# Kernel optimization log

Hardware: AMD Instinct MI355X
Metric: run time of the kernel (lower is better)

The kernel has to match this reference:

```python
import jax, jax.numpy as jnp
import numpy as np

N, E, IN, OUT, ED, NT, H = 20000, 640000, 128, 256, 32, 16, 8
GATC = OUT // 2          # 128 per-layer GAT width
C = GATC // H            # 16 per-head dim
GINEC = OUT - GATC       # 128


def setup_inputs() -> dict:
    key = jax.random.key(0)
    ks = jax.random.split(key, 16)
    s = 0.05
    return {
        "x": jax.random.normal(ks[0], (N, IN), jnp.float32),
        "edge_index": jax.random.randint(ks[1], (2, E), 0, N, jnp.int64),
        "edge_attr": jax.random.normal(ks[2], (E, ED), jnp.float32),
        "edge_types": jax.random.randint(ks[3], (E,), 0, NT, jnp.int64),
        "gat_W": jax.random.normal(ks[4], (IN, H * C), jnp.float32) * s,
        "gat_b": jnp.zeros((H * C,), jnp.float32),
        "gat_edge_W": jax.random.normal(ks[5], (ED, H * C), jnp.float32) * s,
        "gat_a_src": jax.random.normal(ks[6], (H, C), jnp.float32) * s,
        "gat_a_dst": jax.random.normal(ks[7], (H, C), jnp.float32) * s,
        "gat_a_edge": jax.random.normal(ks[8], (H, C), jnp.float32) * s,
        "gat_type_emb": jax.random.normal(ks[9], (NT, ED), jnp.float32) * s,
        "gine_type_emb": jax.random.normal(ks[10], (NT, ED), jnp.float32) * s,
        "gine_edge_W": jax.random.normal(ks[11], (ED, IN), jnp.float32) * s,
        "gine_edge_b": jnp.zeros((IN,), jnp.float32),
        "gine_eps": jnp.zeros((1,), jnp.float32),
        "gine_W1": jax.random.normal(ks[12], (IN, GINEC), jnp.float32) * s,
        "gine_b1": jnp.zeros((GINEC,), jnp.float32),
        "gine_W2": jax.random.normal(ks[13], (GINEC, GINEC), jnp.float32) * s,
        "gine_b2": jnp.zeros((GINEC,), jnp.float32),
        "comb_W": jax.random.normal(ks[14], (H * C + GINEC, OUT), jnp.float32) * s,
        "comb_b": jnp.zeros((OUT,), jnp.float32),
        "ln_g": jnp.ones((OUT,), jnp.float32),
        "ln_b": jnp.zeros((OUT,), jnp.float32),
    }


def reference(x, edge_index, edge_attr, edge_types,
              gat_W, gat_b, gat_edge_W, gat_a_src, gat_a_dst, gat_a_edge,
              gat_type_emb, gine_type_emb, gine_edge_W, gine_edge_b, gine_eps,
              gine_W1, gine_b1, gine_W2, gine_b2, comb_W, comb_b, ln_g, ln_b):
    n = x.shape[0]
    h_, c_ = gat_a_src.shape
    src, dst = edge_index[0], edge_index[1]

    # ---- GAT branch (edge-featured multi-head attention) ----
    e = edge_attr + gat_type_emb[edge_types]                      # [E, ED]
    h = (x @ gat_W).reshape(n, h_, c_)                            # [N, H, C]
    ee = (e @ gat_edge_W).reshape(-1, h_, c_)                     # [E, H, C]
    a_s = jnp.einsum('nhc,hc->nh', h, gat_a_src)                  # [N, H]
    a_d = jnp.einsum('nhc,hc->nh', h, gat_a_dst)
    a_e = jnp.einsum('ehc,hc->eh', ee, gat_a_edge)                # [E, H]
    logit = jax.nn.leaky_relu(a_s[src] + a_d[dst] + a_e, 0.2)     # [E, H]
    # segment softmax over incoming edges of each destination node
    mx = jax.ops.segment_max(logit, dst, num_segments=n)
    p = jnp.exp(logit - mx[dst])
    denom = jax.ops.segment_sum(p, dst, num_segments=n)
    alpha = p / (denom[dst] + 1e-16)                              # [E, H]
    msg = alpha[:, :, None] * h[src]                              # [E, H, C]
    gat_out = jax.ops.segment_sum(msg, dst, num_segments=n).reshape(n, h_ * c_) + gat_b

    # ---- GINE branch ----
    ep = (edge_attr + gine_type_emb[edge_types]) @ gine_edge_W + gine_edge_b  # [E, IN]
    agg = jax.ops.segment_sum(jax.nn.relu(x[src] + ep), dst, num_segments=n)
    h2 = (1.0 + gine_eps[0]) * x + agg
    gine_out = jax.nn.relu(h2 @ gine_W1 + gine_b1) @ gine_W2 + gine_b2        # [N, GINEC]

    # ---- fuse: Linear + LayerNorm + ReLU (dropout is identity in eval) ----
    z = jnp.concatenate([gat_out, gine_out], axis=-1) @ comb_W + comb_b       # [N, OUT]
    mu = jnp.mean(z, axis=-1, keepdims=True)
    var = jnp.var(z, axis=-1, keepdims=True)
    z = (z - mu) * jax.lax.rsqrt(var + 1e-5) * ln_g + ln_b
    return jax.nn.relu(z)
```

## Files before the change

### kernel.cpp

```cpp
#include <hip/hip_runtime.h>

#define N_NODES 20000
#define N_EDGES 640000

typedef _Float16 h2v   __attribute__((ext_vector_type(2)));
typedef _Float16 h16x8 __attribute__((ext_vector_type(8)));
typedef float    f32x4v __attribute__((ext_vector_type(4)));
typedef unsigned u32x4v __attribute__((ext_vector_type(4)));

__device__ __forceinline__ unsigned packh2(float a, float b){
    h2v v; v.x = (_Float16)a; v.y = (_Float16)b;
    return __builtin_bit_cast(unsigned, v);
}

__global__ void k0_zero(float4* __restrict__ p, int n4){
    int i = blockIdx.x*blockDim.x + threadIdx.x;
    int stride = gridDim.x*blockDim.x;
    float4 z; z.x=0.f; z.y=0.f; z.z=0.f; z.w=0.f;
    for (; i<n4; i+=stride) p[i] = z;
}

__global__ void kD_detect(const int* __restrict__ eidx_w, const int* __restrict__ ety_w,
                          int* __restrict__ flags){
    int i = blockIdx.x*blockDim.x + threadIdx.x;
    int stride = gridDim.x*blockDim.x;
    int a0 = 0, a1 = 0;
    for (int w = 2*i+1; w < 2*N_EDGES; w += 2*stride) a0 |= eidx_w[w];
    for (int w = 2*i+1; w < N_EDGES;   w += 2*stride) a1 |= ety_w[w];
    if (a0) atomicOr(&flags[0], 1);
    if (a1) atomicOr(&flags[1], 1);
}

__global__ void kN_norm(const int* __restrict__ eidx_w, const int* __restrict__ ety_w,
                        const int* __restrict__ flags,
                        int* __restrict__ dst, int* __restrict__ srcty,
                        int* __restrict__ rankA, int* __restrict__ cnt){
    int i = blockIdx.x*blockDim.x + threadIdx.x;
    int stride = gridDim.x*blockDim.x;
    const bool e32 = (flags[0] != 0);
    const bool t32 = (flags[1] != 0);
    for (int e = i; e < N_EDGES; e += stride){
        int s, d, t;
        if (e32){ s = eidx_w[e];   d = eidx_w[N_EDGES + e]; }
        else    { s = eidx_w[2*e]; d = eidx_w[2*N_EDGES + 2*e]; }
        t = t32 ? ety_w[e] : ety_w[2*e];
        s = min(max(s, 0), N_NODES-1);
        d = min(max(d, 0), N_NODES-1);
        t = min(max(t, 0), 15);
        dst[e] = d; srcty[e] = s | (t << 20);
        rankA[e] = atomicAdd(&cnt[d], 1);
    }
}

__global__ __launch_bounds__(1024) void kS_scan(const int* __restrict__ cnt,
                                                int* __restrict__ row_ptr){
    __shared__ int sW[16];
    __shared__ int sWS[16];
    __shared__ int sbase;
    const int t = threadIdx.x, lane = t & 63, wv = t >> 6;
    if (t==0) sbase = 0;
    __syncthreads();
    for (int base=0; base<N_NODES; base+=4096){
        const int idx0 = base + t*4;
        int v0 = (idx0  <N_NODES) ? cnt[idx0  ] : 0;
        int v1 = (idx0+1<N_NODES) ? cnt[idx0+1] : 0;
        int v2 = (idx0+2<N_NODES) ? cnt[idx0+2] : 0;
        int v3 = (idx0+3<N_NODES) ? cnt[idx0+3] : 0;
        int p1 = v0+v1, p2 = p1+v2, tot = p2+v3;
        int xs = tot;
        #pragma unroll
        for (int off=1; off<64; off<<=1){
            int y = __shfl_up(xs, off, 64);
            if (lane >= off) xs += y;
        }
        if (lane==63) sW[wv] = xs;
        __syncthreads();
        if (t < 16){
            int wvv = sW[t], ws = wvv;
            #pragma unroll
            for (int off=1; off<16; off<<=1){
                int y = __shfl_up(ws, off, 16);
                if ((t&15) >= off) ws += y;
            }
            sWS[t] = ws - wvv;
        }
        __syncthreads();
        int ex = sbase + sWS[wv] + xs - tot;
        if (idx0  <N_NODES){ row_ptr[idx0  ]=ex;    }
        if (idx0+1<N_NODES){ row_ptr[idx0+1]=ex+v0; }
        if (idx0+2<N_NODES){ row_ptr[idx0+2]=ex+p1; }
        if (idx0+3<N_NODES){ row_ptr[idx0+3]=ex+p2; }
        __syncthreads();
        if (t==0) sbase += sWS[15] + sW[15];
        __syncthreads();
    }
    if (t==0) row_ptr[N_NODES] = sbase;
}

__global__ __launch_bounds__(256) void kPre(const float* __restrict__ gat_edge_W,
                                            const float* __restrict__ a_edge,
                                            const float* __restrict__ gat_emb,
                                            const float* __restrict__ gine_emb,
                                            const float* __restrict__ gine_edge_W,
                                            const float* __restrict__ gine_edge_b,
                                            float* __restrict__ Mt, float* __restrict__ ATw,
                                            float* __restrict__ Tw){
    const int t = threadIdx.x;
    if (blockIdx.x < 16){
        if (t < 128){
            const int tyv = blockIdx.x;
            float acc = gine_edge_b[t];
            #pragma unroll
            for (int d=0;d<32;d++) acc += gine_emb[tyv*32+d]*gine_edge_W[d*128+t];
            Tw[tyv*128+t] = acc;
        }
        return;
    }
    __shared__ float sM[32*8];
    const int d = t>>3, hh = t&7;
    float acc = 0.f;
    #pragma unroll
    for (int c=0;c<16;c++) acc += gat_edge_W[d*128 + hh*16 + c]*a_edge[hh*16 + c];
    sM[d*8+hh] = acc; Mt[hh*32 + d] = acc;
    __syncthreads();
    if (t < 128){
        int tyv = t>>3, h2 = t&7;
        float a = 0.f;
        #pragma unroll
        for (int dd=0;dd<32;dd++) a += gat_emb[tyv*32+dd]*sM[dd*8+h2];
        ATw[tyv*8+h2] = a;
    }
}

__global__ __launch_bounds__(256) void kW_pack(
    const float* __restrict__ W1, const float* __restrict__ W2,
    const float* __restrict__ combW,
    unsigned* __restrict__ W1p, unsigned* __restrict__ W2p, unsigned* __restrict__ combp)
{
    const int tid = blockIdx.x*256 + threadIdx.x;
    const int chunk = tid >> 6;
    const int l = tid & 63;
    const int n = l & 15, g = l >> 4;
    const float* W; unsigned* P; int NCH, cbase;
    if (chunk < 32)      { W = W1;    P = W1p;   NCH = 128; cbase = chunk; }
    else if (chunk < 64) { W = W2;    P = W2p;   NCH = 128; cbase = chunk - 32; }
    else if (chunk < 192){ W = combW; P = combp; NCH = 256; cbase = chunk - 64; }
    else return;
    const int nblocks = NCH/16;
    const int kstep = cbase / nblocks, nblk = cbase % nblocks;
    const int k0 = kstep*32 + 8*g, col = nblk*16 + n;
    unsigned u0 = packh2(W[(size_t)(k0+0)*NCH + col], W[(size_t)(k0+1)*NCH + col]);
    unsigned u1 = packh2(W[(size_t)(k0+2)*NCH + col], W[(size_t)(k0+3)*NCH + col]);
    unsigned u2 = packh2(W[(size_t)(k0+4)*NCH + col], W[(size_t)(k0+5)*NCH + col]);
    unsigned u3 = packh2(W[(size_t)(k0+6)*NCH + col], W[(size_t)(k0+7)*NCH + col]);
    ((uint4*)P)[(size_t)cbase*64 + l] = make_uint4(u0,u1,u2,u3);
}

__global__ __launch_bounds__(128) void k1_node_prep(
    const float* __restrict__ x, const float* __restrict__ gat_W,
    const float* __restrict__ a_src, const float* __restrict__ a_dst,
    unsigned* __restrict__ xhb, float* __restrict__ as_out, float* __restrict__ ad_out)
{
    __shared__ float sX[8][128];
    __shared__ float sH[128];
    const int t = threadIdx.x;
    const int base = blockIdx.x*8;
    const float4* xin = (const float4*)(x + (size_t)base*128);
    float4* sx4 = (float4*)&sX[0][0];
    for (int i=t;i<256;i+=128) sx4[i] = xin[i];
    __syncthreads();
    float acc[8] = {0,0,0,0,0,0,0,0};
    for (int k=0;k<128;k++){
        float w = gat_W[k*128 + t];
        #pragma unroll
        for (int nn=0;nn<8;nn++) acc[nn] += sX[nn][k]*w;
    }
    const float asv = a_src[t], advv = a_dst[t];
    #pragma unroll
    for (int nn=0;nn<8;nn++){
        const int n = base + nn;
        float vs = acc[nn]*asv, vd = acc[nn]*advv;
        #pragma unroll
        for (int off=8; off>=1; off>>=1){ vs += __shfl_xor(vs,off,16); vd += __shfl_xor(vd,off,16); }
        if ((t&15)==0){ as_out[n*8 + (t>>4)] = vs; ad_out[n*8 + (t>>4)] = vd; }
        __syncthreads();
        sH[t] = acc[nn];
        __syncthreads();
        if (t < 64){
            xhb[(size_t)n*128 + t] = packh2(sX[nn][2*t], sX[nn][2*t+1]);
        } else {
            int i = t - 64;
            xhb[(size_t)n*128 + 64 + i] = packh2(sH[2*i], sH[2*i+1]);
        }
    }
}

__global__ __launch_bounds__(256) void kCE_edge(
    const float* __restrict__ eattr,
    const int* __restrict__ dstA, const int* __restrict__ styA,
    const int* __restrict__ rankA, const int* __restrict__ rowp,
    const float* __restrict__ a_s, const float* __restrict__ a_d,
    const float* __restrict__ Mt, const float* __restrict__ ATw,
    const float* __restrict__ gine_emb,
    unsigned* __restrict__ erec)
{
    const int t = threadIdx.x;
    const int q = t & 7;
    float4 mtr[8];
    #pragma unroll
    for (int h=0;h<8;h++) mtr[h] = ((const float4*)Mt)[h*8 + q];

    const int e0 = (blockIdx.x*256 + t) >> 3;
    const int estride = (gridDim.x*256) >> 3;
    for (int e = e0; e < N_EDGES; e += estride){
        float4 f = ((const float4*)eattr)[(size_t)e*8 + q];
        const int d    = dstA[e];
        const int sty  = styA[e];
        const int pos  = rowp[d] + rankA[e];
        const int srcn = sty & 0xFFFFF;
        const int tyv  = ((unsigned)sty)>>20;

        const float4 ge = ((const float4*)gine_emb)[tyv*8 + q];
        ((uint2*)erec)[(size_t)pos*16 + q] =
            make_uint2(packh2(f.x+ge.x, f.y+ge.y), packh2(f.z+ge.z, f.w+ge.w));

        float ph[8];
        #pragma unroll
        for (int h=0;h<8;h++)
            ph[h] = f.x*mtr[h].x + f.y*mtr[h].y + f.z*mtr[h].z + f.w*mtr[h].w;
        #pragma unroll
        for (int i=0;i<4;i++){
            float send = (q&1) ? ph[2*i] : ph[2*i+1];
            float recv = __shfl_xor(send, 1, 64);
            ph[i] = ((q&1) ? ph[2*i+1] : ph[2*i]) + recv;
        }
        #pragma unroll
        for (int i=0;i<2;i++){
            float send = (q&2) ? ph[2*i] : ph[2*i+1];
            float recv = __shfl_xor(send, 2, 64);
            ph[i] = ((q&2) ? ph[2*i+1] : ph[2*i]) + recv;
        }
        {
            float send = (q&4) ? ph[0] : ph[1];
            float recv = __shfl_xor(send, 4, 64);
            ph[0] = ((q&4) ? ph[1] : ph[0]) + recv;
        }

        float lg = a_s[srcn*8+q] + a_d[d*8+q] + ph[0] + ATw[tyv*8+q];
        lg = (lg>0.f) ? lg : 0.2f*lg;
        ((float*)erec)[(size_t)pos*32 + 16 + q] = __expf(lg);
        ((int*)erec)[(size_t)pos*32 + 24 + q] = sty;
    }
}

template<bool MASK>
__device__ __forceinline__ void gine_block16(
    int pos0, int rem, int m, int g,
    const unsigned* __restrict__ xhb, const unsigned* __restrict__ erec,
    const h16x8* aw, const float* bb,
    float* accA, float* accG, float* ps)
{
    const int mc = MASK ? (m < rem ? m : rem - 1) : m;
    u32x4v uu = ((const u32x4v*)erec)[(size_t)(pos0 + mc)*8 + g];
    h16x8 evf = __builtin_bit_cast(h16x8, uu);

    const _Float16* xp[4];
    int ecl[4];
    #pragma unroll
    for (int r=0;r<4;r++){
        const int er = 4*g + r;
        const int ec = MASK ? (er < rem ? er : rem - 1) : er;
        ecl[r] = pos0 + ec;
        const int srcn = ((const int*)erec)[(size_t)(pos0 + ec)*32 + 24] & 0xFFFFF;
        xp[r] = (const _Float16*)(xhb + (size_t)srcn*128) + m;
    }
    #pragma unroll
    for (int hf4=0; hf4<2; hf4++){
        f32x4v pv[4];
        #pragma unroll
        for (int r=0;r<4;r++){
            pv[r] = *(const f32x4v*)((const float*)erec + (size_t)ecl[r]*32 + 16 + hf4*4);
            if (MASK && (4*g + r) >= rem) pv[r] = (f32x4v){0.f,0.f,0.f,0.f};
        }
        #pragma unroll
        for (int r=0;r<4;r++){
            ps[hf4*4+0] += pv[r][0]; ps[hf4*4+1] += pv[r][1];
            ps[hf4*4+2] += pv[r][2]; ps[hf4*4+3] += pv[r][3];
        }
        #pragma unroll
        for (int cc=0; cc<4; cc++){
            const int c = hf4*4 + cc;
            f32x4v Dv = { bb[c], bb[c], bb[c], bb[c] };
            Dv = __builtin_amdgcn_mfma_f32_16x16x32_f16(evf, aw[c], Dv, 0, 0, 0);
            #pragma unroll
            for (int r=0;r<4;r++){
                float xf = (float)xp[r][c*16];
                float hf = (float)xp[r][128 + c*16];
                float tmp = fmaxf(xf + Dv[r], 0.f);
                if (MASK && (4*g + r) >= rem) tmp = 0.f;
                accA[c] += tmp;
                accG[c] += pv[r][cc] * hf;
            }
        }
    }
}

__global__ __launch_bounds__(256) void k3_gather(
    const unsigned* __restrict__ xhb, const unsigned* __restrict__ erec,
    const int* __restrict__ row_ptr,
    const float* __restrict__ gine_b, const float* __restrict__ gine_W,
    float* __restrict__ agg, float* __restrict__ gacc)
{
    const int t = threadIdx.x;
    const int lane = t & 63;
    const int m = lane & 15;
    const int g = lane >> 4;

    h16x8 aw[8];
    #pragma unroll
    for (int c=0;c<8;c++){
        #pragma unroll
        for (int j=0;j<8;j++)
            aw[c][j] = (_Float16)gine_W[(8*g + j)*128 + c*16 + m];
    }
    float bb[8];
    #pragma unroll
    for (int c=0;c<8;c++) bb[c] = gine_b[c*16 + m];

    const int nwaves = gridDim.x*4;
    for (int d = blockIdx.x*4 + (t>>6); d < N_NODES; d += nwaves){
        const int row = row_ptr[d], end = row_ptr[d+1];
        float accA[8] = {0,0,0,0,0,0,0,0};
        float accG[8] = {0,0,0,0,0,0,0,0};
        float ps[8]   = {0,0,0,0,0,0,0,0};
        const int deg = end - row;
        int pos0 = row;
        const int nfull = deg >> 4;
        for (int b=0;b<nfull;b++, pos0+=16)
            gine_block16<false>(pos0, 16, m, g, xhb, erec, aw, bb, accA, accG, ps);
        const int rem = deg & 15;
        if (rem)
            gine_block16<true>(pos0, rem, m, g, xhb, erec, aw, bb, accA, accG, ps);
        #pragma unroll
        for (int c=0;c<8;c++){
            accA[c] += __shfl_xor(accA[c], 16, 64);
            accA[c] += __shfl_xor(accA[c], 32, 64);
            accG[c] += __shfl_xor(accG[c], 16, 64);
            accG[c] += __shfl_xor(accG[c], 32, 64);
            ps[c]   += __shfl_xor(ps[c],   16, 64);
            ps[c]   += __shfl_xor(ps[c],   32, 64);
        }
        if (g == 0){
            #pragma unroll
            for (int c=0;c<8;c++){
                const float inv = 1.f/(ps[c] + 1e-16f);
                agg [(size_t)d*128 + c*16 + m] = accA[c];
                gacc[(size_t)d*128 + c*16 + m] = accG[c]*inv;
            }
        }
    }
}

#define K4N 32
__global__ __launch_bounds__(256) void k4_final(
    const float* __restrict__ x, const float* __restrict__ agg, const float* __restrict__ gacc,
    const float* __restrict__ gat_b, const float* __restrict__ eps_p,
    const unsigned* __restrict__ W1p, const float* __restrict__ b1,
    const unsigned* __restrict__ W2p, const float* __restrict__ gb2,
    const unsigned* __restrict__ combp, const float* __restrict__ comb_b,
    const float* __restrict__ ln_g, const float* __restrict__ ln_b,
    float* __restrict__ out)
{
    __shared__ _Float16 sHi[K4N][136];
    __shared__ _Float16 sLo[K4N][136];
    __shared__ _Float16 sCH[K4N][264];
    __shared__ float sRed[K4N][8];
    __shared__ float sMV[K4N][2];
    const int t = threadIdx.x;
    const int l = t & 63, wid = t >> 6;
    const int n = l & 15, g = l >> 4;
    const float epsv = 1.f + eps_p[0];
    const int base = blockIdx.x*K4N;

    for (int i = t; i < K4N*32; i += 256){
        const int node = i >> 5, c4 = i & 31;
        float4 xv = ((const float4*)x   )[(size_t)(base+node)*32 + c4];
        float4 av = ((const float4*)agg )[(size_t)(base+node)*32 + c4];
        float4 gv = ((const float4*)gacc)[(size_t)(base+node)*32 + c4];
        float4 bv = ((const float4*)gat_b)[c4];
        float h0 = epsv*xv.x + av.x, h1 = epsv*xv.y + av.y;
        float h2_ = epsv*xv.z + av.z, h3 = epsv*xv.w + av.w;
        _Float16 f0=(_Float16)h0, f1=(_Float16)h1, f2=(_Float16)h2_, f3=(_Float16)h3;
        h2v p01; p01.x=f0; p01.y=f1;  h2v p23; p23.x=f2; p23.y=f3;
        *(uint2*)&sHi[node][c4*4] = make_uint2(__builtin_bit_cast(unsigned,p01),
                                               __builtin_bit_cast(unsigned,p23));
        h2v q01, q23;
        q01.x=(_Float16)(h0-(float)f0); q01.y=(_Float16)(h1-(float)f1);
        q23.x=(_Float16)(h2_-(float)f2); q23.y=(_Float16)(h3-(float)f3);
        *(uint2*)&sLo[node][c4*4] = make_uint2(__builtin_bit_cast(unsigned,q01),
                                               __builtin_bit_cast(unsigned,q23));
        *(uint2*)&sCH[node][c4*4] = make_uint2(packh2(gv.x+bv.x, gv.y+bv.y),
                                               packh2(gv.z+bv.z, gv.w+bv.w));
    }
    __syncthreads();

    f32x4v acc1[2][2];
    #pragma unroll
    for (int mt=0;mt<2;mt++)
        #pragma unroll
        for (int nt=0;nt<2;nt++){
            float b = b1[32*wid + 16*nt + n];
            acc1[mt][nt] = (f32x4v){b,b,b,b};
        }
    #pragma unroll
    for (int ks=0;ks<4;ks++){
        h16x8 bfr[2];
        #pragma unroll
        for (int nt=0;nt<2;nt++){
            uint4 u = ((const uint4*)W1p)[(size_t)((ks*8 + 2*wid + nt)*64 + l)];
            bfr[nt] = __builtin_bit_cast(h16x8, u);
        }
        #pragma unroll
        for (int mt=0;mt<2;mt++){
            const int row = 16*mt + n;
            h16x8 ahi = *(const h16x8*)&sHi[row][8*g + 32*ks];
            h16x8 alo = *(const h16x8*)&sLo[row][8*g + 32*ks];
            #pragma unroll
            for (int nt=0;nt<2;nt++){
                acc1[mt][nt] = __builtin_amdgcn_mfma_f32_16x16x32_f16(ahi, bfr[nt], acc1[mt][nt], 0,0,0);
                acc1[mt][nt] = __builtin_amdgcn_mfma_f32_16x16x32_f16(alo, bfr[nt], acc1[mt][nt], 0,0,0);
            }
        }
    }
    __syncthreads();
    #pragma unroll
    for (int mt=0;mt<2;mt++)
        #pragma unroll
        for (int nt=0;nt<2;nt++)
            #pragma unroll
            for (int r=0;r<4;r++)
                sHi[16*mt + 4*g + r][32*wid + 16*nt + n] = (_Float16)fmaxf(acc1[mt][nt][r], 0.f);
    __syncthreads();

    f32x4v acc2[2][2];
    #pragma unroll
    for (int mt=0;mt<2;mt++)
        #pragma unroll
        for (int nt=0;nt<2;nt++){
            float b = gb2[32*wid + 16*nt + n];
            acc2[mt][nt] = (f32x4v){b,b,b,b};
        }
    #pragma unroll
    for (int ks=0;ks<4;ks++){
        h16x8 bfr[2];
        #pragma unroll
        for (int nt=0;nt<2;nt++){
            uint4 u = ((const uint4*)W2p)[(size_t)((ks*8 + 2*wid + nt)*64 + l)];
            bfr[nt] = __builtin_bit_cast(h16x8, u);
        }
        #pragma unroll
        for (int mt=0;mt<2;mt++){
            h16x8 a = *(const h16x8*)&sHi[16*mt + n][8*g + 32*ks];
            #pragma unroll
            for (int nt=0;nt<2;nt++)
                acc2[mt][nt] = __builtin_amdgcn_mfma_f32_16x16x32_f16(a, bfr[nt], acc2[mt][nt], 0,0,0);
        }
    }
    #pragma unroll
    for (int mt=0;mt<2;mt++)
        #pragma unroll
        for (int nt=0;nt<2;nt++)
            #pragma unroll
            for (int r=0;r<4;r++)
                sCH[16*mt + 4*g + r][128 + 32*wid + 16*nt + n] = (_Float16)acc2[mt][nt][r];
    __syncthreads();

    f32x4v accC[2][4];
    #pragma unroll
    for (int mt=0;mt<2;mt++)
        #pragma unroll
        for (int nt=0;nt<4;nt++){
            float b = comb_b[64*wid + 16*nt + n];
            accC[mt][nt] = (f32x4v){b,b,b,b};
        }
    #pragma unroll
    for (int ks=0;ks<8;ks++){
        h16x8 bfr[4];
        #pragma unroll
        for (int nt=0;nt<4;nt++){
            uint4 u = ((const uint4*)combp)[(size_t)((ks*16 + 4*wid + nt)*64 + l)];
            bfr[nt] = __builtin_bit_cast(h16x8, u);
        }
        #pragma unroll
        for (int mt=0;mt<2;mt++){
            h16x8 a = *(const h16x8*)&sCH[16*mt + n][8*g + 32*ks];
            #pragma unroll
            for (int nt=0;nt<4;nt++)
                accC[mt][nt] = __builtin_amdgcn_mfma_f32_16x16x32_f16(a, bfr[nt], accC[mt][nt], 0,0,0);
        }
    }

    #pragma unroll
    for (int mt=0;mt<2;mt++)
        #pragma unroll
        for (int r=0;r<4;r++){
            float s1=0.f, s2=0.f;
            #pragma unroll
            for (int nt=0;nt<4;nt++){ float z = accC[mt][nt][r]; s1 += z; s2 += z*z; }
            #pragma unroll
            for (int off=1; off<16; off<<=1){ s1 += __shfl_xor(s1,off,16); s2 += __shfl_xor(s2,off,16); }
            if (n==0){
                sRed[16*mt + 4*g + r][2*wid  ] = s1;
                sRed[16*mt + 4*g + r][2*wid+1] = s2;
            }
        }
    __syncthreads();
    if (t < K4N){
        float a1 = sRed[t][0]+sRed[t][2]+sRed[t][4]+sRed[t][6];
        float a2 = sRed[t][1]+sRed[t][3]+sRed[t][5]+sRed[t][7];
        float mu = a1*(1.f/256.f);
        float var = a2*(1.f/256.f) - mu*mu;
        sMV[t][0] = mu; sMV[t][1] = rsqrtf(var + 1e-5f);
    }
    __syncthreads();
    float lg[4], lb[4];
    #pragma unroll
    for (int nt=0;nt<4;nt++){ int ch = 64*wid + 16*nt + n; lg[nt]=ln_g[ch]; lb[nt]=ln_b[ch]; }
    #pragma unroll
    for (int mt=0;mt<2;mt++)
        #pragma unroll
        for (int r=0;r<4;r++){
            const int row = 16*mt + 4*g + r;
            const float mu = sMV[row][0], rs = sMV[row][1];
            #pragma unroll
            for (int nt=0;nt<4;nt++){
                const int ch = 64*wid + 16*nt + n;
                float zz = accC[mt][nt][r];
                out[(size_t)(base+row)*256 + ch] = fmaxf((zz-mu)*rs*lg[nt] + lb[nt], 0.f);
            }
        }
}

extern "C" void kernel_launch(void* const* d_in, const int* in_sizes, int n_in,
                              void* d_out, int out_size, void* d_ws, size_t ws_size,
                              hipStream_t stream)
{
    (void)in_sizes; (void)n_in; (void)out_size; (void)ws_size;
    const float* x           = (const float*)d_in[0];
    const int*   eidx_w      = (const int*)  d_in[1];
    const float* eattr       = (const float*)d_in[2];
    const int*   ety_w       = (const int*)  d_in[3];
    const float* gat_W       = (const float*)d_in[4];
    const float* gat_b       = (const float*)d_in[5];
    const float* gat_edge_W  = (const float*)d_in[6];
    const float* a_src       = (const float*)d_in[7];
    const float* a_dst       = (const float*)d_in[8];
    const float* a_edge      = (const float*)d_in[9];
    const float* gat_emb     = (const float*)d_in[10];
    const float* gine_emb    = (const float*)d_in[11];
    const float* gine_edge_W = (const float*)d_in[12];
    const float* gine_edge_b = (const float*)d_in[13];
    const float* gine_eps    = (const float*)d_in[14];
    const float* W1          = (const float*)d_in[15];
    const float* b1          = (const float*)d_in[16];
    const float* W2          = (const float*)d_in[17];
    const float* gb2         = (const float*)d_in[18];
    const float* comb_W      = (const float*)d_in[19];
    const float* comb_b      = (const float*)d_in[20];
    const float* ln_g        = (const float*)d_in[21];
    const float* ln_b        = (const float*)d_in[22];
    float* out = (float*)d_out;

    char* ws = (char*)d_ws;
    size_t off = 0;
    auto alloc = [&](size_t bytes)->void*{ void* p = ws + off; off += (bytes + 255)/256*256; return p; };
    size_t zero_start = off;
    int*      flags  = (int*)     alloc(256);
    int*      cnt    = (int*)     alloc((size_t)N_NODES*4);
    size_t zero_bytes = off - zero_start;
    int*      dstA   = (int*)     alloc((size_t)N_EDGES*4);
    int*      styA   = (int*)     alloc((size_t)N_EDGES*4);
    int*      rankA  = (int*)     alloc((size_t)N_EDGES*4);
    int*      rowp   = (int*)     alloc((size_t)(N_NODES+1)*4);
    unsigned* erec   = (unsigned*)alloc((size_t)N_EDGES*128);
    unsigned* xhb    = (unsigned*)alloc((size_t)N_NODES*128*4);
    float*    a_s    = (float*)   alloc((size_t)N_NODES*8*4);
    float*    a_d    = (float*)   alloc((size_t)N_NODES*8*4);
    float*    Mt     = (float*)   alloc(32*8*4);
    float*    ATw    = (float*)   alloc(16*8*4);
    float*    Tw     = (float*)   alloc(16*128*4);
    float*    agg    = (float*)   alloc((size_t)N_NODES*128*4);
    float*    gacc   = (float*)   alloc((size_t)N_NODES*128*4);
    unsigned* W1p    = (unsigned*)alloc((size_t)32*1024);
    unsigned* W2p    = (unsigned*)alloc((size_t)32*1024);
    unsigned* combp  = (unsigned*)alloc((size_t)128*1024);

    int n4 = (int)(zero_bytes/16);
    k0_zero<<<(n4+255)/256, 256, 0, stream>>>((float4*)(ws + zero_start), n4);
    kD_detect<<<512, 256, 0, stream>>>(eidx_w, ety_w, flags);
    kN_norm<<<1024, 256, 0, stream>>>(eidx_w, ety_w, flags, dstA, styA, rankA, cnt);
    kS_scan<<<1, 1024, 0, stream>>>(cnt, rowp);

    kW_pack<<<48, 256, 0, stream>>>(W1, W2, comb_W, W1p, W2p, combp);
    kPre<<<17, 256, 0, stream>>>(gat_edge_W, a_edge, gat_emb, gine_emb,
                                 gine_edge_W, gine_edge_b, Mt, ATw, Tw);
    k1_node_prep<<<N_NODES/8, 128, 0, stream>>>(x, gat_W, a_src, a_dst, xhb, a_s, a_d);

    kCE_edge<<<2500, 256, 0, stream>>>(eattr, dstA, styA, rankA, rowp,
                                       a_s, a_d, Mt, ATw, gine_emb, erec);

    k3_gather<<<2500, 256, 0, stream>>>(xhb, erec, rowp,
                                        gine_edge_b, gine_edge_W, agg, gacc);

    k4_final<<<N_NODES/K4N, 256, 0, stream>>>(x, agg, gacc, gat_b, gine_eps,
                                              W1p, b1, W2p, gb2, combp, comb_b,
                                              ln_g, ln_b, out);
}
```

Baseline: 422.8 us.

## Remap gather lanes to adjacent column pairs for packed half2 loads

```diff
diff --git a/kernel.cpp b/kernel.cpp
--- a/kernel.cpp
+++ b/kernel.cpp
@@ -248,59 +248,57 @@
 
         float lg = a_s[srcn*8+q] + a_d[d*8+q] + ph[0] + ATw[tyv*8+q];
         lg = (lg>0.f) ? lg : 0.2f*lg;
-        ((float*)erec)[(size_t)pos*32 + 16 + q] = __expf(lg);
+        ((float*)erec)[(size_t)pos*32 + 16 + ((q&1)*4 + (q>>1))] = __expf(lg);
         ((int*)erec)[(size_t)pos*32 + 24 + q] = sty;
     }
 }
 
 template<bool MASK>
 __device__ __forceinline__ void gine_block16(
-    int pos0, int rem, int m, int g,
+    int pos0, int rem, int lm, int g,
     const unsigned* __restrict__ xhb, const unsigned* __restrict__ erec,
-    const h16x8* aw, const float* bb,
-    float* accA, float* accG, float* ps)
+    const h16x8* awe, const h16x8* awo, const float* be, const float* bo,
+    float* accA0, float* accA1, float* accG0, float* accG1, float* ps)
 {
-    const int mc = MASK ? (m < rem ? m : rem - 1) : m;
+    const int mc = MASK ? (lm < rem ? lm : rem - 1) : lm;
     u32x4v uu = ((const u32x4v*)erec)[(size_t)(pos0 + mc)*8 + g];
     h16x8 evf = __builtin_bit_cast(h16x8, uu);
-
-    const _Float16* xp[4];
-    int ecl[4];
+    const int P = lm >> 3;
+
+    const unsigned* xq[4];
+    f32x4v pv[4];
     #pragma unroll
     for (int r=0;r<4;r++){
         const int er = 4*g + r;
         const int ec = MASK ? (er < rem ? er : rem - 1) : er;
-        ecl[r] = pos0 + ec;
-        const int srcn = ((const int*)erec)[(size_t)(pos0 + ec)*32 + 24] & 0xFFFFF;
-        xp[r] = (const _Float16*)(xhb + (size_t)srcn*128) + m;
-    }
-    #pragma unroll
-    for (int hf4=0; hf4<2; hf4++){
-        f32x4v pv[4];
+        const int pe = pos0 + ec;
+        const int srcn = ((const int*)erec)[(size_t)pe*32 + 24] & 0xFFFFF;
+        xq[r] = xhb + (size_t)srcn*128;
+        pv[r] = *(const f32x4v*)((const float*)erec + (size_t)pe*32 + 16 + P*4);
+        if (MASK && er >= rem) pv[r] = (f32x4v){0.f,0.f,0.f,0.f};
+    }
+    #pragma unroll
+    for (int r=0;r<4;r++){
+        ps[0] += pv[r][0]; ps[1] += pv[r][1]; ps[2] += pv[r][2]; ps[3] += pv[r][3];
+    }
+    #pragma unroll
+    for (int c=0;c<4;c++){
+        f32x4v De = { be[c], be[c], be[c], be[c] };
+        f32x4v Do = { bo[c], bo[c], bo[c], bo[c] };
+        De = __builtin_amdgcn_mfma_f32_16x16x32_f16(evf, awe[c], De, 0, 0, 0);
+        Do = __builtin_amdgcn_mfma_f32_16x16x32_f16(evf, awo[c], Do, 0, 0, 0);
         #pragma unroll
         for (int r=0;r<4;r++){
-            pv[r] = *(const f32x4v*)((const float*)erec + (size_t)ecl[r]*32 + 16 + hf4*4);
-            if (MASK && (4*g + r) >= rem) pv[r] = (f32x4v){0.f,0.f,0.f,0.f};
-        }
-        #pragma unroll
-        for (int r=0;r<4;r++){
-            ps[hf4*4+0] += pv[r][0]; ps[hf4*4+1] += pv[r][1];
-            ps[hf4*4+2] += pv[r][2]; ps[hf4*4+3] += pv[r][3];
-        }
-        #pragma unroll
-        for (int cc=0; cc<4; cc++){
-            const int c = hf4*4 + cc;
-            f32x4v Dv = { bb[c], bb[c], bb[c], bb[c] };
-            Dv = __builtin_amdgcn_mfma_f32_16x16x32_f16(evf, aw[c], Dv, 0, 0, 0);
-            #pragma unroll
-            for (int r=0;r<4;r++){
-                float xf = (float)xp[r][c*16];
-                float hf = (float)xp[r][128 + c*16];
-                float tmp = fmaxf(xf + Dv[r], 0.f);
-                if (MASK && (4*g + r) >= rem) tmp = 0.f;
-                accA[c] += tmp;
-                accG[c] += pv[r][cc] * hf;
-            }
+            const unsigned xw = xq[r][16*c + lm];
+            const unsigned hw = xq[r][64 + 16*c + lm];
+            h2v xv = __builtin_bit_cast(h2v, xw);
+            h2v hv = __builtin_bit_cast(h2v, hw);
+            float a0 = fmaxf(De[r] + (float)xv.x, 0.f);
+            float a1 = fmaxf(Do[r] + (float)xv.y, 0.f);
+            if (MASK && (4*g + r) >= rem){ a0 = 0.f; a1 = 0.f; }
+            accA0[c] += a0; accA1[c] += a1;
+            accG0[c] += pv[r][c]*(float)hv.x;
+            accG1[c] += pv[r][c]*(float)hv.y;
         }
     }
 }
@@ -313,49 +311,52 @@
 {
     const int t = threadIdx.x;
     const int lane = t & 63;
-    const int m = lane & 15;
+    const int lm = lane & 15;
     const int g = lane >> 4;
 
-    h16x8 aw[8];
-    #pragma unroll
-    for (int c=0;c<8;c++){
-        #pragma unroll
-        for (int j=0;j<8;j++)
-            aw[c][j] = (_Float16)gine_W[(8*g + j)*128 + c*16 + m];
-    }
-    float bb[8];
-    #pragma unroll
-    for (int c=0;c<8;c++) bb[c] = gine_b[c*16 + m];
+    h16x8 awe[4], awo[4];
+    #pragma unroll
+    for (int c=0;c<4;c++){
+        #pragma unroll
+        for (int j=0;j<8;j++){
+            awe[c][j] = (_Float16)gine_W[(8*g + j)*128 + 32*c + 2*lm];
+            awo[c][j] = (_Float16)gine_W[(8*g + j)*128 + 32*c + 2*lm + 1];
+        }
+    }
+    float be[4], bo[4];
+    #pragma unroll
+    for (int c=0;c<4;c++){ be[c] = gine_b[32*c + 2*lm]; bo[c] = gine_b[32*c + 2*lm + 1]; }
 
     const int nwaves = gridDim.x*4;
     for (int d = blockIdx.x*4 + (t>>6); d < N_NODES; d += nwaves){
         const int row = row_ptr[d], end = row_ptr[d+1];
-        float accA[8] = {0,0,0,0,0,0,0,0};
-        float accG[8] = {0,0,0,0,0,0,0,0};
-        float ps[8]   = {0,0,0,0,0,0,0,0};
+        float accA0[4]={0,0,0,0}, accA1[4]={0,0,0,0};
+        float accG0[4]={0,0,0,0}, accG1[4]={0,0,0,0};
+        float ps[4]={0,0,0,0};
         const int deg = end - row;
         int pos0 = row;
         const int nfull = deg >> 4;
         for (int b=0;b<nfull;b++, pos0+=16)
-            gine_block16<false>(pos0, 16, m, g, xhb, erec, aw, bb, accA, accG, ps);
+            gine_block16<false>(pos0, 16, lm, g, xhb, erec, awe, awo, be, bo,
+                                accA0, accA1, accG0, accG1, ps);
         const int rem = deg & 15;
         if (rem)
-            gine_block16<true>(pos0, rem, m, g, xhb, erec, aw, bb, accA, accG, ps);
-        #pragma unroll
-        for (int c=0;c<8;c++){
-            accA[c] += __shfl_xor(accA[c], 16, 64);
-            accA[c] += __shfl_xor(accA[c], 32, 64);
-            accG[c] += __shfl_xor(accG[c], 16, 64);
-            accG[c] += __shfl_xor(accG[c], 32, 64);
-            ps[c]   += __shfl_xor(ps[c],   16, 64);
-            ps[c]   += __shfl_xor(ps[c],   32, 64);
+            gine_block16<true>(pos0, rem, lm, g, xhb, erec, awe, awo, be, bo,
+                               accA0, accA1, accG0, accG1, ps);
+        #pragma unroll
+        for (int c=0;c<4;c++){
+            accA0[c] += __shfl_xor(accA0[c], 16, 64); accA0[c] += __shfl_xor(accA0[c], 32, 64);
+            accA1[c] += __shfl_xor(accA1[c], 16, 64); accA1[c] += __shfl_xor(accA1[c], 32, 64);
+            accG0[c] += __shfl_xor(accG0[c], 16, 64); accG0[c] += __shfl_xor(accG0[c], 32, 64);
+            accG1[c] += __shfl_xor(accG1[c], 16, 64); accG1[c] += __shfl_xor(accG1[c], 32, 64);
+            ps[c]    += __shfl_xor(ps[c],    16, 64); ps[c]    += __shfl_xor(ps[c],    32, 64);
         }
         if (g == 0){
             #pragma unroll
-            for (int c=0;c<8;c++){
+            for (int c=0;c<4;c++){
                 const float inv = 1.f/(ps[c] + 1e-16f);
-                agg [(size_t)d*128 + c*16 + m] = accA[c];
-                gacc[(size_t)d*128 + c*16 + m] = accG[c]*inv;
+                ((float2*)agg )[(size_t)d*64 + 16*c + lm] = make_float2(accA0[c], accA1[c]);
+                ((float2*)gacc)[(size_t)d*64 + 16*c + lm] = make_float2(accG0[c]*inv, accG1[c]*inv);
             }
         }
     }
@@ -609,7 +610,7 @@
     kCE_edge<<<2500, 256, 0, stream>>>(eattr, dstA, styA, rankA, rowp,
                                        a_s, a_d, Mt, ATw, gine_emb, erec);
 
-    k3_gather<<<2500, 256, 0, stream>>>(xhb, erec, rowp,
+    k3_gather<<<5000, 256, 0, stream>>>(xhb, erec, rowp,
                                         gine_edge_b, gine_edge_W, agg, gacc);
 
     k4_final<<<N_NODES/K4N, 256, 0, stream>>>(x, agg, gacc, gat_b, gine_eps,
```

Measured after the change: 500.5 us. 18.4% more time.

## Compute node GAT projection with fp16 MFMA using hi/lo split of x

Applied to the files above, without the earlier changes.

```diff
diff --git a/kernel.cpp b/kernel.cpp
--- a/kernel.cpp
+++ b/kernel.cpp
@@ -134,8 +134,9 @@
 
 __global__ __launch_bounds__(256) void kW_pack(
     const float* __restrict__ W1, const float* __restrict__ W2,
-    const float* __restrict__ combW,
-    unsigned* __restrict__ W1p, unsigned* __restrict__ W2p, unsigned* __restrict__ combp)
+    const float* __restrict__ combW, const float* __restrict__ gatW,
+    unsigned* __restrict__ W1p, unsigned* __restrict__ W2p,
+    unsigned* __restrict__ combp, unsigned* __restrict__ Wgp)
 {
     const int tid = blockIdx.x*256 + threadIdx.x;
     const int chunk = tid >> 6;
@@ -145,6 +146,7 @@
     if (chunk < 32)      { W = W1;    P = W1p;   NCH = 128; cbase = chunk; }
     else if (chunk < 64) { W = W2;    P = W2p;   NCH = 128; cbase = chunk - 32; }
     else if (chunk < 192){ W = combW; P = combp; NCH = 256; cbase = chunk - 64; }
+    else if (chunk < 224){ W = gatW;  P = Wgp;   NCH = 128; cbase = chunk - 192; }
     else return;
     const int nblocks = NCH/16;
     const int kstep = cbase / nblocks, nblk = cbase % nblocks;
@@ -156,42 +158,86 @@
     ((uint4*)P)[(size_t)cbase*64 + l] = make_uint4(u0,u1,u2,u3);
 }
 
-__global__ __launch_bounds__(128) void k1_node_prep(
-    const float* __restrict__ x, const float* __restrict__ gat_W,
+#define K1N 32
+__global__ __launch_bounds__(256) void k1_node_prep(
+    const float* __restrict__ x, const unsigned* __restrict__ Wgp,
     const float* __restrict__ a_src, const float* __restrict__ a_dst,
     unsigned* __restrict__ xhb, float* __restrict__ as_out, float* __restrict__ ad_out)
 {
-    __shared__ float sX[8][128];
-    __shared__ float sH[128];
+    __shared__ _Float16 sXhi[K1N][136];
+    __shared__ _Float16 sXlo[K1N][136];
+    __shared__ float sH[K1N][132];
     const int t = threadIdx.x;
-    const int base = blockIdx.x*8;
-    const float4* xin = (const float4*)(x + (size_t)base*128);
-    float4* sx4 = (float4*)&sX[0][0];
-    for (int i=t;i<256;i+=128) sx4[i] = xin[i];
-    __syncthreads();
-    float acc[8] = {0,0,0,0,0,0,0,0};
-    for (int k=0;k<128;k++){
-        float w = gat_W[k*128 + t];
-        #pragma unroll
-        for (int nn=0;nn<8;nn++) acc[nn] += sX[nn][k]*w;
-    }
-    const float asv = a_src[t], advv = a_dst[t];
-    #pragma unroll
-    for (int nn=0;nn<8;nn++){
-        const int n = base + nn;
-        float vs = acc[nn]*asv, vd = acc[nn]*advv;
-        #pragma unroll
-        for (int off=8; off>=1; off>>=1){ vs += __shfl_xor(vs,off,16); vd += __shfl_xor(vd,off,16); }
-        if ((t&15)==0){ as_out[n*8 + (t>>4)] = vs; ad_out[n*8 + (t>>4)] = vd; }
-        __syncthreads();
-        sH[t] = acc[nn];
-        __syncthreads();
-        if (t < 64){
-            xhb[(size_t)n*128 + t] = packh2(sX[nn][2*t], sX[nn][2*t+1]);
-        } else {
-            int i = t - 64;
-            xhb[(size_t)n*128 + 64 + i] = packh2(sH[2*i], sH[2*i+1]);
-        }
+    const int l = t & 63, wid = t >> 6;
+    const int n = l & 15, g = l >> 4;
+    const int base = blockIdx.x*K1N;
+
+    for (int i = t; i < K1N*32; i += 256){
+        const int node = i >> 5, c4 = i & 31;
+        float4 xv = ((const float4*)x)[(size_t)(base+node)*32 + c4];
+        _Float16 f0=(_Float16)xv.x, f1=(_Float16)xv.y, f2=(_Float16)xv.z, f3=(_Float16)xv.w;
+        h2v p01; p01.x=f0; p01.y=f1;  h2v p23; p23.x=f2; p23.y=f3;
+        unsigned u01 = __builtin_bit_cast(unsigned,p01);
+        unsigned u23 = __builtin_bit_cast(unsigned,p23);
+        *(uint2*)&sXhi[node][c4*4] = make_uint2(u01,u23);
+        h2v q01,q23;
+        q01.x=(_Float16)(xv.x-(float)f0); q01.y=(_Float16)(xv.y-(float)f1);
+        q23.x=(_Float16)(xv.z-(float)f2); q23.y=(_Float16)(xv.w-(float)f3);
+        *(uint2*)&sXlo[node][c4*4] = make_uint2(__builtin_bit_cast(unsigned,q01),
+                                                __builtin_bit_cast(unsigned,q23));
+        ((uint2*)xhb)[(size_t)(base+node)*64 + c4] = make_uint2(u01,u23);
+    }
+    __syncthreads();
+
+    f32x4v acc[2][2];
+    #pragma unroll
+    for (int mt=0;mt<2;mt++)
+        #pragma unroll
+        for (int nt=0;nt<2;nt++) acc[mt][nt] = (f32x4v){0.f,0.f,0.f,0.f};
+    #pragma unroll
+    for (int ks=0;ks<4;ks++){
+        h16x8 bfr[2];
+        #pragma unroll
+        for (int nt=0;nt<2;nt++){
+            uint4 u = ((const uint4*)Wgp)[(size_t)((ks*8 + 2*wid + nt)*64 + l)];
+            bfr[nt] = __builtin_bit_cast(h16x8, u);
+        }
+        #pragma unroll
+        for (int mt=0;mt<2;mt++){
+            const int row = 16*mt + n;
+            h16x8 ahi = *(const h16x8*)&sXhi[row][8*g + 32*ks];
+            h16x8 alo = *(const h16x8*)&sXlo[row][8*g + 32*ks];
+            #pragma unroll
+            for (int nt=0;nt<2;nt++){
+                acc[mt][nt] = __builtin_amdgcn_mfma_f32_16x16x32_f16(ahi, bfr[nt], acc[mt][nt], 0,0,0);
+                acc[mt][nt] = __builtin_amdgcn_mfma_f32_16x16x32_f16(alo, bfr[nt], acc[mt][nt], 0,0,0);
+            }
+        }
+    }
+    #pragma unroll
+    for (int mt=0;mt<2;mt++)
+        #pragma unroll
+        for (int nt=0;nt<2;nt++)
+            #pragma unroll
+            for (int r=0;r<4;r++)
+                sH[16*mt + 4*g + r][32*wid + 16*nt + n] = acc[mt][nt][r];
+    __syncthreads();
+
+    for (int i = t; i < K1N*64; i += 256){
+        const int node = i >> 6, w = i & 63;
+        xhb[(size_t)(base+node)*128 + 64 + w] = packh2(sH[node][2*w], sH[node][2*w+1]);
+    }
+    {
+        const int node = t >> 3, head = t & 7;
+        float vs = 0.f, vd = 0.f;
+        #pragma unroll
+        for (int j=0;j<16;j++){
+            float hv = sH[node][head*16 + j];
+            vs += hv*a_src[head*16 + j];
+            vd += hv*a_dst[head*16 + j];
+        }
+        as_out[(size_t)(base+node)*8 + head] = vs;
+        ad_out[(size_t)(base+node)*8 + head] = vd;
     }
 }
 
@@ -594,6 +640,7 @@
     unsigned* W1p    = (unsigned*)alloc((size_t)32*1024);
     unsigned* W2p    = (unsigned*)alloc((size_t)32*1024);
     unsigned* combp  = (unsigned*)alloc((size_t)128*1024);
+    unsigned* Wgp    = (unsigned*)alloc((size_t)32*1024);
 
     int n4 = (int)(zero_bytes/16);
     k0_zero<<<(n4+255)/256, 256, 0, stream>>>((float4*)(ws + zero_start), n4);
@@ -601,10 +648,10 @@
     kN_norm<<<1024, 256, 0, stream>>>(eidx_w, ety_w, flags, dstA, styA, rankA, cnt);
     kS_scan<<<1, 1024, 0, stream>>>(cnt, rowp);
 
-    kW_pack<<<48, 256, 0, stream>>>(W1, W2, comb_W, W1p, W2p, combp);
+    kW_pack<<<56, 256, 0, stream>>>(W1, W2, comb_W, gat_W, W1p, W2p, combp, Wgp);
     kPre<<<17, 256, 0, stream>>>(gat_edge_W, a_edge, gat_emb, gine_emb,
                                  gine_edge_W, gine_edge_b, Mt, ATw, Tw);
-    k1_node_prep<<<N_NODES/8, 128, 0, stream>>>(x, gat_W, a_src, a_dst, xhb, a_s, a_d);
+    k1_node_prep<<<N_NODES/K1N, 256, 0, stream>>>(x, Wgp, a_src, a_dst, xhb, a_s, a_d);
 
     kCE_edge<<<2500, 256, 0, stream>>>(eattr, dstA, styA, rankA, rowp,
                                        a_s, a_d, Mt, ATw, gine_emb, erec);
```

Result: faster. 405.8 us (-4.0%).
